# Performance work log

Hardware: AMD Instinct MI355X
Metric: run time of the kernel (lower is better)

The kernel has to match this reference:

```python
import math
import jax, jax.numpy as jnp
import numpy as np

B, N, D, H = 8, 512, 1024, 16
HD = D // H
K_DEFAULT, K_MAX, PROX_THR = 8, 12, 20.0


def setup_inputs() -> dict:
    key = jax.random.key(0)
    ks = jax.random.split(key, 12)
    tokens_B = jax.random.normal(ks[0], (B, N, D), dtype=jnp.float32)
    ego_distances = jax.random.uniform(ks[1], (B, N), dtype=jnp.float32)
    ego_mask = jnp.zeros((B, N), dtype=bool).at[:, 0].set(True)  # token 0 is ego
    ego_speed = jax.random.uniform(ks[2], (B,), dtype=jnp.float32)
    s = 1.0 / math.sqrt(D)
    Wq = jax.random.normal(ks[3], (D, D), jnp.float32) * s
    Wk = jax.random.normal(ks[4], (D, D), jnp.float32) * s
    Wv = jax.random.normal(ks[5], (D, D), jnp.float32) * s
    Weq = jax.random.normal(ks[6], (D, D), jnp.float32) * s
    Wo = jax.random.normal(ks[7], (D, D), jnp.float32) * (0.02 * s)
    Dm = D // 4
    W1 = jax.random.normal(ks[8], (Dm, 2), jnp.float32) * (1.0 / math.sqrt(2))
    b1 = jnp.zeros((Dm,), jnp.float32)
    W2 = jax.random.normal(ks[9], (H, Dm), jnp.float32) * (1.0 / math.sqrt(Dm))
    b2 = jnp.zeros((H,), jnp.float32)
    return dict(tokens_B=tokens_B, ego_distances=ego_distances, ego_mask=ego_mask,
                ego_speed=ego_speed, Wq=Wq, Wk=Wk, Wv=Wv, Weq=Weq, Wo=Wo,
                W1=W1, b1=b1, W2=W2, b2=b2)


def _compute_K(ego_speed, ego_distances):
    # deterministic, no-grad lookup (torch: @torch.no_grad)
    n = ego_distances.shape[1]
    close = (ego_distances < PROX_THR).astype(jnp.float32).sum(-1)
    density = close / max(n, 1)
    avg_speed = float(jnp.mean(ego_speed))
    avg_density = float(jnp.mean(density))
    K = K_DEFAULT
    if avg_speed > 15.0:
        K = min(K + 1, K_MAX)
    if avg_density > 0.5:
        K = min(K + 1, K_MAX)
    return min(K, n - 1)


def reference(tokens_B, ego_distances, ego_mask, ego_speed, Wq, Wk, Wv, Weq, Wo, W1, b1, W2, b2):
    b, n, d = tokens_B.shape
    K = _compute_K(ego_speed, ego_distances)
    if K <= 0:
        return jnp.zeros_like(tokens_B)

    # top-K nearest-to-ego neighbors per token, excluding self
    eye = jnp.eye(n, dtype=bool)
    dist_rank = jnp.where(eye[None, :, :], jnp.inf, ego_distances[:, None, :])  # (B,N,N)
    _, topk_idx = jax.lax.top_k(-dist_rank, K)  # (B,N,K) indices of smallest dists

    neighbors = jax.vmap(lambda t, idx: t[idx])(tokens_B, topk_idx)  # (B,N,K,D)

    is_ego = ego_mask.astype(tokens_B.dtype)[..., None]
    Q = (1.0 - is_ego) * (tokens_B @ Wq.T) + is_ego * (tokens_B @ Weq.T)
    Km = neighbors @ Wk.T
    Vm = neighbors @ Wv.T

    Q = Q.reshape(b, n, H, HD).transpose(0, 2, 1, 3)              # (B,H,N,hd)
    Km = Km.reshape(b, n, K, H, HD).transpose(0, 3, 1, 2, 4)      # (B,H,N,K,hd)
    Vm = Vm.reshape(b, n, K, H, HD).transpose(0, 3, 1, 2, 4)

    scores = jnp.einsum('bhnd,bhnkd->bhnk', Q, Km) / math.sqrt(HD)

    # additive pairwise distance bias MLP on (d_i_to_ego, d_j_to_ego)
    d_i = jnp.broadcast_to(ego_distances[:, :, None], (b, n, K))
    d_j = jax.vmap(lambda dd, idx: dd[idx])(ego_distances, topk_idx)
    dist_pair = jnp.stack([d_i, d_j], axis=-1)                    # (B,N,K,2)
    bias = jax.nn.relu(dist_pair @ W1.T + b1) @ W2.T + b2         # (B,N,K,H)
    scores = scores + bias.transpose(0, 3, 1, 2)                  # FIX-1: additive

    attn = jax.nn.softmax(scores, axis=-1)
    out = jnp.einsum('bhnk,bhnkd->bhnd', attn, Vm)
    out = out.transpose(0, 2, 1, 3).reshape(b, n, d)              # FIX-2 axis order
    return out @ Wo.T
```

## Files before the change

### kernel.cpp

```cpp
#include <hip/hip_runtime.h>
#include <math.h>

#define Bn 8
#define Nn 512
#define Dn 1024
#define Hn 16
#define HDn 64
#define KMAX 12
#define NSMAX 13
#define PROX 20.0f

typedef __attribute__((ext_vector_type(8))) short bf16x8;
typedef __attribute__((ext_vector_type(4))) float f32x4;

__device__ __forceinline__ unsigned short f2bf(float f) {
    unsigned int u = __float_as_uint(f);
    return (unsigned short)((u + 0x7FFFu + ((u >> 16) & 1u)) >> 16);
}

__global__ __launch_bounds__(256) void cvt_meta_kernel(const float* __restrict__ tokens,
                                                       const float* __restrict__ Wq,
                                                       const float* __restrict__ Wo,
                                                       const float* __restrict__ Wk,
                                                       const float* __restrict__ Wv,
                                                       const float* __restrict__ dist,
                                                       const float* __restrict__ speed,
                                                       unsigned short* __restrict__ tok_h,
                                                       unsigned short* __restrict__ wq_h,
                                                       unsigned short* __restrict__ wo_h,
                                                       unsigned short* __restrict__ wkv_h,
                                                       int* __restrict__ meta,
                                                       int* __restrict__ Lidx,
                                                       unsigned short* __restrict__ tok_g) {
    int blk = blockIdx.x;
    if (blk < 8192) {
        const float* src;
        unsigned short* dst;
        int local;
        if (blk < 4096) { src = tokens; dst = tok_h; local = blk; }
        else if (blk < 5120) { src = Wq; dst = wq_h; local = blk - 4096; }
        else if (blk < 6144) { src = Wo; dst = wo_h; local = blk - 5120; }
        else if (blk < 7168) { src = Wk; dst = wkv_h; local = blk - 6144; }
        else { src = Wv; dst = wkv_h + (size_t)Dn * Dn; local = blk - 7168; }
        int i = (local * 256 + threadIdx.x) * 4;
        float4 v = *(const float4*)&src[i];
        ushort4 o;
        o.x = f2bf(v.x); o.y = f2bf(v.y); o.z = f2bf(v.z); o.w = f2bf(v.w);
        *(ushort4*)&dst[i] = o;
        return;
    }
    if (threadIdx.x >= 64) return;
    int lane = threadIdx.x;
    int b = blk - 8192;

    int cnt = 0;
    for (int i = lane; i < Bn * Nn; i += 64) cnt += (dist[i] < PROX) ? 1 : 0;
    for (int off = 32; off; off >>= 1) cnt += __shfl_xor(cnt, off);

    float sp = 0.f;
    for (int i = lane; i < Bn; i += 64) sp += speed[i];
    for (int off = 32; off; off >>= 1) sp += __shfl_xor(sp, off);

    float avg_density = (float)cnt / (float)(Bn * Nn);
    float avg_speed = sp / (float)Bn;
    int K = 8;
    if (avg_speed > 15.0f) K = min(K + 1, KMAX);
    if (avg_density > 0.5f) K = min(K + 1, KMAX);
    K = min(K, Nn - 1);
    if (b == 0 && lane == 0) meta[0] = K;
    int ns = K + 1;

    int sel[NSMAX];
    float dloc[Nn / 64];
    #pragma unroll
    for (int j = 0; j < Nn / 64; ++j) dloc[j] = dist[b * Nn + lane + 64 * j];
    for (int r = 0; r < ns; ++r) {
        float mv = 1e30f;
        int mi = 0;
        #pragma unroll
        for (int j = 0; j < Nn / 64; ++j) {
            if (dloc[j] < mv) { mv = dloc[j]; mi = lane + 64 * j; }
        }
        for (int off = 32; off; off >>= 1) {
            float ov = __shfl_xor(mv, off);
            int oi = __shfl_xor(mi, off);
            if (ov < mv || (ov == mv && oi < mi)) { mv = ov; mi = oi; }
        }
        sel[r] = mi;
        if (lane == 0) Lidx[b * NSMAX + r] = mi;
        if ((mi & 63) == lane) dloc[mi >> 6] = 1e30f;
    }

    const float* srcp = &tokens[(size_t)(b * Nn + sel[0]) * Dn];
    float4 pre[4];
    #pragma unroll
    for (int q = 0; q < 4; ++q) pre[q] = *(const float4*)&srcp[(q * 64 + lane) * 4];
    for (int s = 0; s < ns; ++s) {
        float4 cur[4];
        #pragma unroll
        for (int q = 0; q < 4; ++q) cur[q] = pre[q];
        if (s + 1 < ns) {
            srcp = &tokens[(size_t)(b * Nn + sel[s + 1]) * Dn];
            #pragma unroll
            for (int q = 0; q < 4; ++q) pre[q] = *(const float4*)&srcp[(q * 64 + lane) * 4];
        }
        unsigned short* dst = &tok_g[(size_t)(b * 16 + s) * Dn];
        #pragma unroll
        for (int q = 0; q < 4; ++q) {
            ushort4 o;
            o.x = f2bf(cur[q].x); o.y = f2bf(cur[q].y); o.z = f2bf(cur[q].z); o.w = f2bf(cur[q].w);
            *(ushort4*)&dst[(q * 64 + lane) * 4] = o;
        }
    }
}

__device__ __forceinline__ void gemm_body_s(const unsigned short* A,
                                            const unsigned short* Bm,
                                            float* Cf, unsigned short* Ch,
                                            int Nd, int Kd, int sA, int sB,
                                            int bm, int bn, int mode, int hh,
                                            unsigned short* As, unsigned short* Bs) {
    int t = threadIdx.x;
    int wave = t >> 6, lane = t & 63;
    int wm = wave >> 1, wn = wave & 1;

    int srow = lane >> 2;
    int skoff = (lane & 3) * 8;
    const unsigned short* Ag  = A  + (size_t)(bm + wave * 16 + srow) * sA + skoff;
    const unsigned short* Bg  = Bm + (size_t)(bn + wave * 32 + srow) * sB + skoff;
    const unsigned short* Bg2 = Bg + (size_t)16 * sB;

    f32x4 acc[2][4] = {};
    int fm = lane & 15;
    int fk = (lane >> 4) * 8;

    auto stage = [&](int buf) {
        unsigned short* AsW  = As + buf * 2048 + (wave * 16) * 32;
        unsigned short* BsW  = Bs + buf * 4096 + (wave * 32) * 32;
        __builtin_amdgcn_global_load_lds((const __attribute__((address_space(1))) void*)Ag,
                                         (__attribute__((address_space(3))) void*)AsW, 16, 0, 0);
        __builtin_amdgcn_global_load_lds((const __attribute__((address_space(1))) void*)Bg,
                                         (__attribute__((address_space(3))) void*)BsW, 16, 0, 0);
        __builtin_amdgcn_global_load_lds((const __attribute__((address_space(1))) void*)Bg2,
                                         (__attribute__((address_space(3))) void*)(BsW + 512), 16, 0, 0);
        Ag += 32; Bg += 32; Bg2 += 32;
    };

    int nsteps = Kd >> 5;
    stage(0);
    __syncthreads();
    int cur = 0;
    for (int s = 0; s < nsteps; ++s) {
        if (s + 1 < nsteps) stage(cur ^ 1);
        const unsigned short* Ab = As + cur * 2048;
        const unsigned short* Bb = Bs + cur * 4096;
        bf16x8 af[2], bfr[4];
        #pragma unroll
        for (int mi = 0; mi < 2; ++mi)
            af[mi] = *(const bf16x8*)&Ab[(wm * 32 + mi * 16 + fm) * 32 + fk];
        #pragma unroll
        for (int ni = 0; ni < 4; ++ni)
            bfr[ni] = *(const bf16x8*)&Bb[(wn * 64 + ni * 16 + fm) * 32 + fk];
        #pragma unroll
        for (int mi = 0; mi < 2; ++mi)
            #pragma unroll
            for (int ni = 0; ni < 4; ++ni)
                acc[mi][ni] = __builtin_amdgcn_mfma_f32_16x16x32_bf16(af[mi], bfr[ni], acc[mi][ni], 0, 0, 0);
        __syncthreads();
        cur ^= 1;
    }

    int erow = (lane >> 4) * 4;
    #pragma unroll
    for (int mi = 0; mi < 2; ++mi)
        #pragma unroll
        for (int ni = 0; ni < 4; ++ni)
            #pragma unroll
            for (int r = 0; r < 4; ++r) {
                int row = bm + wm * 32 + mi * 16 + erow + r;
                int col = bn + wn * 64 + ni * 16 + fm;
                if (mode == 0) {
                    Cf[(size_t)row * Nd + col] = acc[mi][ni][r];
                } else if (mode == 1) {
                    Ch[(size_t)row * Nd + col] = f2bf(acc[mi][ni][r]);
                } else {
                    int bb = col >> 4, ss = col & 15;
                    Ch[((size_t)bb * 1024 + row) * 256 + ss * 16 + hh] = f2bf(acc[mi][ni][r]);
                }
            }
}

__global__ __launch_bounds__(256) void proj_fused_kernel(const unsigned short* __restrict__ tok_h,
                                                         const unsigned short* __restrict__ wq_h,
                                                         const unsigned short* __restrict__ tok_g,
                                                         const unsigned short* __restrict__ wkv_h,
                                                         const float* __restrict__ tokens,
                                                         const float* __restrict__ Weq,
                                                         float* __restrict__ Qbuf,
                                                         float* __restrict__ Kproj,
                                                         unsigned short* __restrict__ v_h,
                                                         float* __restrict__ Qego) {
    __shared__ unsigned short As[2 * 64 * 32];
    __shared__ unsigned short Bs[2 * 128 * 32];
    __shared__ float tok[Dn];

    int blk = blockIdx.x;
    if (blk < 16) {
        gemm_body_s(tok_g, wkv_h, Kproj, 0, Dn, Dn, Dn, Dn,
                    (blk >> 3) * 64, (blk & 7) * 128, 0, 0, As, Bs);
    } else if (blk < 32) {
        int idx = blk - 16;
        gemm_body_s(tok_g, wkv_h + (size_t)Dn * Dn, 0, v_h, Dn, Dn, Dn, Dn,
                    (idx >> 3) * 64, (idx & 7) * 128, 1, 0, As, Bs);
    } else if (blk < 544) {
        int idx = blk - 32;
        gemm_body_s(tok_h, wq_h, Qbuf, 0, Dn, Dn, Dn, Dn,
                    (idx >> 3) * 64, (idx & 7) * 128, 0, 0, As, Bs);
    } else {
        int blk2 = blk - 544;
        int b = blk2 >> 5, cg = blk2 & 31;
        for (int t = threadIdx.x; t < Dn; t += 256) tok[t] = tokens[(size_t)(b * Nn) * Dn + t];
        __syncthreads();
        int w = threadIdx.x >> 6, lane = threadIdx.x & 63;
        for (int o = 0; o < 8; ++o) {
            int col = cg * 32 + w * 8 + o;
            const float* wr = &Weq[(size_t)col * Dn];
            float sum = 0.f;
            #pragma unroll
            for (int q = 0; q < 4; ++q) {
                float4 w4 = *(const float4*)&wr[q * 256 + lane * 4];
                float4 t4 = *(const float4*)&tok[q * 256 + lane * 4];
                sum += w4.x * t4.x + w4.y * t4.y + w4.z * t4.z + w4.w * t4.w;
            }
            for (int off = 32; off; off >>= 1) sum += __shfl_xor(sum, off);
            if (lane == 0) Qego[(size_t)b * Dn + col] = sum;
        }
    }
}

__global__ __launch_bounds__(256) void vo3_gemm_kernel(const unsigned short* __restrict__ wo_h,
                                                       const unsigned short* __restrict__ v_h,
                                                       unsigned short* __restrict__ Vo3T) {
    __shared__ unsigned short As[2 * 64 * 32];
    __shared__ unsigned short Bs[2 * 128 * 32];
    int h = blockIdx.y;
    gemm_body_s(wo_h + h * HDn, v_h + h * HDn, 0, Vo3T, 0, HDn, Dn, Dn,
                blockIdx.x * 64, 0, 2, h, As, Bs);
}

#define HSTR 264
__global__ __launch_bounds__(256) void attn_kernel(const float* __restrict__ Q,
                                                   const float* __restrict__ Qego,
                                                   const float* __restrict__ Kproj,
                                                   const float* __restrict__ dist,
                                                   const float* __restrict__ W1,
                                                   const float* __restrict__ b1,
                                                   const float* __restrict__ W2,
                                                   const float* __restrict__ b2,
                                                   const int* __restrict__ meta,
                                                   const int* __restrict__ Lidx,
                                                   unsigned short* __restrict__ Wt) {
    __shared__ float hid[KMAX * HSTR];
    __shared__ float sc[Hn * NSMAX];
    __shared__ float at[Hn * NSMAX];
    __shared__ int selslot[NSMAX];
    __shared__ int inv[16];
    __shared__ float dj[NSMAX];

    int bi = blockIdx.x;
    int b = bi >> 9;
    int i = bi & (Nn - 1);
    int K = meta[0];
    int ns = K + 1;
    int t = threadIdx.x;
    int g = t >> 4, l = t & 15;

    float d_i = dist[b * Nn + i];

    const float* qsrc = (i == 0) ? &Qego[(size_t)b * Dn] : &Q[(size_t)bi * Dn];
    float4 qv = *(const float4*)&qsrc[g * HDn + l * 4];
    float4 w2v[4];
    #pragma unroll
    for (int ii = 0; ii < 4; ++ii)
        w2v[ii] = *(const float4*)&W2[g * 256 + ii * 64 + l * 4];

    if (t < 64) {
        int s = t;
        int jj = (s < ns) ? Lidx[b * NSMAX + s] : -1;
        bool valid = (s < ns) && (jj != i);
        unsigned long long mask = __ballot(valid);
        int rank = __popcll(mask & ((1ull << s) - 1ull));
        bool take = valid && (rank < K);
        if (take) {
            selslot[rank] = s;
            dj[rank] = dist[b * Nn + jj];
        }
        if (s < 16) inv[s] = take ? rank : -1;
    }
    __syncthreads();

    {
        float2 w01 = *(const float2*)&W1[2 * t];
        float bb = b1[t];
        for (int k = 0; k < K; ++k) {
            float h = w01.x * d_i + w01.y * dj[k] + bb;
            hid[k * HSTR + t] = h > 0.f ? h : 0.f;
        }
    }
    __syncthreads();

    {
        float bias0 = b2[g];
        float4 kvn = *(const float4*)&Kproj[(size_t)(b * 16 + selslot[0]) * Dn + g * HDn + l * 4];
        for (int k = 0; k < K; ++k) {
            float4 kv4 = kvn;
            if (k + 1 < K)
                kvn = *(const float4*)&Kproj[(size_t)(b * 16 + selslot[k + 1]) * Dn + g * HDn + l * 4];
            float val = (qv.x * kv4.x + qv.y * kv4.y + qv.z * kv4.z + qv.w * kv4.w) * 0.125f;
            #pragma unroll
            for (int ii = 0; ii < 4; ++ii) {
                float4 h4 = *(const float4*)&hid[k * HSTR + ii * 64 + l * 4];
                val += w2v[ii].x * h4.x + w2v[ii].y * h4.y + w2v[ii].z * h4.z + w2v[ii].w * h4.w;
            }
            val += __shfl_xor(val, 1);
            val += __shfl_xor(val, 2);
            val += __shfl_xor(val, 4);
            val += __shfl_xor(val, 8);
            if (l == 0) sc[g * NSMAX + k] = val + bias0;
        }
    }
    __syncthreads();

    {
        int k = l;
        float s = (k < K) ? sc[g * NSMAX + k] : -1e30f;
        float m = s;
        m = fmaxf(m, __shfl_xor(m, 1));
        m = fmaxf(m, __shfl_xor(m, 2));
        m = fmaxf(m, __shfl_xor(m, 4));
        m = fmaxf(m, __shfl_xor(m, 8));
        float e = (k < K) ? expf(s - m) : 0.f;
        float ssum = e;
        ssum += __shfl_xor(ssum, 1);
        ssum += __shfl_xor(ssum, 2);
        ssum += __shfl_xor(ssum, 4);
        ssum += __shfl_xor(ssum, 8);
        if (k < K) at[g * NSMAX + k] = e / ssum;
    }
    __syncthreads();

    {
        int s = t >> 4, h = t & 15;
        int k = (s < NSMAX) ? inv[s] : -1;
        float a = (k >= 0) ? at[h * NSMAX + k] : 0.f;
        Wt[(size_t)bi * 256 + t] = f2bf(a);
    }
}

__global__ __launch_bounds__(256) void final_gemm_kernel(const unsigned short* __restrict__ Wt,
                                                         const unsigned short* __restrict__ Vo3T,
                                                         float* __restrict__ out) {
    __shared__ unsigned short As[2 * 64 * 32];
    __shared__ unsigned short Bs[2 * 128 * 32];
    int rbase = blockIdx.y * 64;
    int b = rbase >> 9;
    int bmloc = rbase & (Nn - 1);
    gemm_body_s(Wt + (size_t)b * Nn * 256,
                Vo3T + (size_t)b * Dn * 256,
                out + (size_t)b * Nn * Dn, 0,
                Dn, 256, 256, 256, bmloc, blockIdx.x * 128, 0, 0, As, Bs);
}

extern "C" void kernel_launch(void* const* d_in, const int* in_sizes, int n_in,
                              void* d_out, int out_size, void* d_ws, size_t ws_size,
                              hipStream_t stream) {
    (void)in_sizes; (void)n_in; (void)out_size; (void)ws_size;
    const float* tokens = (const float*)d_in[0];
    const float* dist   = (const float*)d_in[1];
    const float* speed  = (const float*)d_in[3];
    const float* Wq  = (const float*)d_in[4];
    const float* Wk  = (const float*)d_in[5];
    const float* Wv  = (const float*)d_in[6];
    const float* Weq = (const float*)d_in[7];
    const float* Wo  = (const float*)d_in[8];
    const float* W1  = (const float*)d_in[9];
    const float* b1  = (const float*)d_in[10];
    const float* W2  = (const float*)d_in[11];
    const float* b2  = (const float*)d_in[12];
    float* out = (float*)d_out;

    char* ws = (char*)d_ws;
    const size_t SZ_KP   = (size_t)128 * Dn * sizeof(float);
    const size_t SZ_VH   = (size_t)128 * Dn * sizeof(unsigned short);
    const size_t SZ_V3   = (size_t)Bn * Dn * 256 * sizeof(unsigned short);
    const size_t SZ_WT   = (size_t)Bn * Nn * 256 * sizeof(unsigned short);
    const size_t SZ_BIG  = (size_t)Bn * Nn * Dn * sizeof(float);
    const size_t SZ_BIGH = (size_t)Bn * Nn * Dn * sizeof(unsigned short);
    const size_t SZ_WH   = (size_t)Dn * Dn * sizeof(unsigned short);
    const size_t SZ_TG   = (size_t)128 * Dn * sizeof(unsigned short);
    const size_t SZ_QE   = (size_t)Bn * Dn * sizeof(float);

    size_t off = 0;
    int*   meta  = (int*)(ws + off);  off += 256;
    int*   Lidx  = (int*)(ws + off);  off += 768;
    float* Kproj = (float*)(ws + off); off += SZ_KP;
    float* Qbuf  = (float*)(ws + off); off += SZ_BIG;
    float* Qego  = (float*)(ws + off); off += SZ_QE;
    unsigned short* v_h   = (unsigned short*)(ws + off); off += SZ_VH;
    unsigned short* Vo3T  = (unsigned short*)(ws + off); off += SZ_V3;
    unsigned short* Wt    = (unsigned short*)(ws + off); off += SZ_WT;
    unsigned short* tok_h = (unsigned short*)(ws + off); off += SZ_BIGH;
    unsigned short* wq_h  = (unsigned short*)(ws + off); off += SZ_WH;
    unsigned short* wo_h  = (unsigned short*)(ws + off); off += SZ_WH;
    unsigned short* wkv_h = (unsigned short*)(ws + off); off += 2 * SZ_WH;
    unsigned short* tok_g = (unsigned short*)(ws + off); off += SZ_TG;

    cvt_meta_kernel<<<8200, 256, 0, stream>>>(tokens, Wq, Wo, Wk, Wv, dist, speed,
                                              tok_h, wq_h, wo_h, wkv_h, meta, Lidx, tok_g);
    proj_fused_kernel<<<800, 256, 0, stream>>>(tok_h, wq_h, tok_g, wkv_h, tokens, Weq,
                                               Qbuf, Kproj, v_h, Qego);
    vo3_gemm_kernel<<<dim3(16, 16), 256, 0, stream>>>(wo_h, v_h, Vo3T);
    attn_kernel<<<Bn * Nn, 256, 0, stream>>>(Qbuf, Qego, Kproj, dist, W1, b1, W2, b2,
                                             meta, Lidx, Wt);
    final_gemm_kernel<<<dim3(Dn / 128, (Bn * Nn) / 64), 256, 0, stream>>>(Wt, Vo3T, out);
}
```

Before: 177.4 us.

## Store Q projection in bf16 and run attention with one wavefront per token

The Q projection GEMM now writes bf16 output instead of fp32, halving the Q buffer written by the projection and read by the attention kernel. The attention kernel is shrunk from 256 threads to a single 64-lane wavefront per token, which loops over heads and hidden units and drops all block barriers. It also switches to fast __expf and vectorized ushort4 stores of the attention weights. The risk is reduced Q precision and less parallelism per block, since each lane now handles four heads serially.

```diff
diff --git a/kernel.cpp b/kernel.cpp
--- a/kernel.cpp
+++ b/kernel.cpp
@@ -16,6 +16,9 @@
 __device__ __forceinline__ unsigned short f2bf(float f) {
     unsigned int u = __float_as_uint(f);
     return (unsigned short)((u + 0x7FFFu + ((u >> 16) & 1u)) >> 16);
+}
+__device__ __forceinline__ float bf2f(unsigned short u) {
+    return __uint_as_float(((unsigned int)u) << 16);
 }
 
 __global__ __launch_bounds__(256) void cvt_meta_kernel(const float* __restrict__ tokens,
@@ -196,7 +199,7 @@
                                                          const unsigned short* __restrict__ wkv_h,
                                                          const float* __restrict__ tokens,
                                                          const float* __restrict__ Weq,
-                                                         float* __restrict__ Qbuf,
+                                                         unsigned short* __restrict__ Qbuf_h,
                                                          float* __restrict__ Kproj,
                                                          unsigned short* __restrict__ v_h,
                                                          float* __restrict__ Qego) {
@@ -214,8 +217,8 @@
                     (idx >> 3) * 64, (idx & 7) * 128, 1, 0, As, Bs);
     } else if (blk < 544) {
         int idx = blk - 32;
-        gemm_body_s(tok_h, wq_h, Qbuf, 0, Dn, Dn, Dn, Dn,
-                    (idx >> 3) * 64, (idx & 7) * 128, 0, 0, As, Bs);
+        gemm_body_s(tok_h, wq_h, 0, Qbuf_h, Dn, Dn, Dn, Dn,
+                    (idx >> 3) * 64, (idx & 7) * 128, 1, 0, As, Bs);
     } else {
         int blk2 = blk - 544;
         int b = blk2 >> 5, cg = blk2 & 31;
@@ -249,17 +252,17 @@
 }
 
 #define HSTR 264
-__global__ __launch_bounds__(256) void attn_kernel(const float* __restrict__ Q,
-                                                   const float* __restrict__ Qego,
-                                                   const float* __restrict__ Kproj,
-                                                   const float* __restrict__ dist,
-                                                   const float* __restrict__ W1,
-                                                   const float* __restrict__ b1,
-                                                   const float* __restrict__ W2,
-                                                   const float* __restrict__ b2,
-                                                   const int* __restrict__ meta,
-                                                   const int* __restrict__ Lidx,
-                                                   unsigned short* __restrict__ Wt) {
+__global__ __launch_bounds__(64) void attn_kernel(const unsigned short* __restrict__ Qh,
+                                                  const float* __restrict__ Qego,
+                                                  const float* __restrict__ Kproj,
+                                                  const float* __restrict__ dist,
+                                                  const float* __restrict__ W1,
+                                                  const float* __restrict__ b1,
+                                                  const float* __restrict__ W2,
+                                                  const float* __restrict__ b2,
+                                                  const int* __restrict__ meta,
+                                                  const int* __restrict__ Lidx,
+                                                  unsigned short* __restrict__ Wt) {
     __shared__ float hid[KMAX * HSTR];
     __shared__ float sc[Hn * NSMAX];
     __shared__ float at[Hn * NSMAX];
@@ -272,20 +275,13 @@
     int i = bi & (Nn - 1);
     int K = meta[0];
     int ns = K + 1;
-    int t = threadIdx.x;
-    int g = t >> 4, l = t & 15;
+    int lane = threadIdx.x;
+    int gq = lane >> 4, l = lane & 15;
 
     float d_i = dist[b * Nn + i];
 
-    const float* qsrc = (i == 0) ? &Qego[(size_t)b * Dn] : &Q[(size_t)bi * Dn];
-    float4 qv = *(const float4*)&qsrc[g * HDn + l * 4];
-    float4 w2v[4];
-    #pragma unroll
-    for (int ii = 0; ii < 4; ++ii)
-        w2v[ii] = *(const float4*)&W2[g * 256 + ii * 64 + l * 4];
-
-    if (t < 64) {
-        int s = t;
+    {
+        int s = lane;
         int jj = (s < ns) ? Lidx[b * NSMAX + s] : -1;
         bool valid = (s < ns) && (jj != i);
         unsigned long long mask = __ballot(valid);
@@ -297,20 +293,33 @@
         }
         if (s < 16) inv[s] = take ? rank : -1;
     }
-    __syncthreads();
-
-    {
-        float2 w01 = *(const float2*)&W1[2 * t];
-        float bb = b1[t];
+
+    #pragma unroll
+    for (int j = 0; j < 4; ++j) {
+        int c = lane + 64 * j;
+        float2 w01 = *(const float2*)&W1[2 * c];
+        float bb = b1[c];
         for (int k = 0; k < K; ++k) {
             float h = w01.x * d_i + w01.y * dj[k] + bb;
-            hid[k * HSTR + t] = h > 0.f ? h : 0.f;
-        }
-    }
-    __syncthreads();
-
-    {
+            hid[k * HSTR + c] = h > 0.f ? h : 0.f;
+        }
+    }
+
+    for (int gg = 0; gg < 4; ++gg) {
+        int g = gq * 4 + gg;
+        float4 qv;
+        if (i == 0) {
+            qv = *(const float4*)&Qego[(size_t)b * Dn + g * HDn + l * 4];
+        } else {
+            ushort4 qh = *(const ushort4*)&Qh[(size_t)bi * Dn + g * HDn + l * 4];
+            qv.x = bf2f(qh.x); qv.y = bf2f(qh.y); qv.z = bf2f(qh.z); qv.w = bf2f(qh.w);
+        }
+        float4 w2v[4];
+        #pragma unroll
+        for (int ii = 0; ii < 4; ++ii)
+            w2v[ii] = *(const float4*)&W2[g * 256 + ii * 64 + l * 4];
         float bias0 = b2[g];
+
         float4 kvn = *(const float4*)&Kproj[(size_t)(b * 16 + selslot[0]) * Dn + g * HDn + l * 4];
         for (int k = 0; k < K; ++k) {
             float4 kv4 = kvn;
@@ -329,31 +338,38 @@
             if (l == 0) sc[g * NSMAX + k] = val + bias0;
         }
     }
-    __syncthreads();
-
-    {
+
+    #pragma unroll
+    for (int hh = 0; hh < 4; ++hh) {
+        int h = gq * 4 + hh;
         int k = l;
-        float s = (k < K) ? sc[g * NSMAX + k] : -1e30f;
+        float s = (k < K) ? sc[h * NSMAX + k] : -1e30f;
         float m = s;
         m = fmaxf(m, __shfl_xor(m, 1));
         m = fmaxf(m, __shfl_xor(m, 2));
         m = fmaxf(m, __shfl_xor(m, 4));
         m = fmaxf(m, __shfl_xor(m, 8));
-        float e = (k < K) ? expf(s - m) : 0.f;
+        float e = (k < K) ? __expf(s - m) : 0.f;
         float ssum = e;
         ssum += __shfl_xor(ssum, 1);
         ssum += __shfl_xor(ssum, 2);
         ssum += __shfl_xor(ssum, 4);
         ssum += __shfl_xor(ssum, 8);
-        if (k < K) at[g * NSMAX + k] = e / ssum;
-    }
-    __syncthreads();
+        if (k < K) at[h * NSMAX + k] = e / ssum;
+    }
 
     {
-        int s = t >> 4, h = t & 15;
-        int k = (s < NSMAX) ? inv[s] : -1;
-        float a = (k >= 0) ? at[h * NSMAX + k] : 0.f;
-        Wt[(size_t)bi * 256 + t] = f2bf(a);
+        ushort4 o;
+        unsigned short* op = (unsigned short*)&o;
+        #pragma unroll
+        for (int j = 0; j < 4; ++j) {
+            int tt = lane * 4 + j;
+            int s = tt >> 4, h = tt & 15;
+            int k = (s < NSMAX) ? inv[s] : -1;
+            float a = (k >= 0) ? at[h * NSMAX + k] : 0.f;
+            op[j] = f2bf(a);
+        }
+        *(ushort4*)&Wt[(size_t)bi * 256 + lane * 4] = o;
     }
 }
 
@@ -394,7 +410,7 @@
     const size_t SZ_VH   = (size_t)128 * Dn * sizeof(unsigned short);
     const size_t SZ_V3   = (size_t)Bn * Dn * 256 * sizeof(unsigned short);
     const size_t SZ_WT   = (size_t)Bn * Nn * 256 * sizeof(unsigned short);
-    const size_t SZ_BIG  = (size_t)Bn * Nn * Dn * sizeof(float);
+    const size_t SZ_QH   = (size_t)Bn * Nn * Dn * sizeof(unsigned short);
     const size_t SZ_BIGH = (size_t)Bn * Nn * Dn * sizeof(unsigned short);
     const size_t SZ_WH   = (size_t)Dn * Dn * sizeof(unsigned short);
     const size_t SZ_TG   = (size_t)128 * Dn * sizeof(unsigned short);
@@ -404,8 +420,8 @@
     int*   meta  = (int*)(ws + off);  off += 256;
     int*   Lidx  = (int*)(ws + off);  off += 768;
     float* Kproj = (float*)(ws + off); off += SZ_KP;
-    float* Qbuf  = (float*)(ws + off); off += SZ_BIG;
     float* Qego  = (float*)(ws + off); off += SZ_QE;
+    unsigned short* Qbuf_h = (unsigned short*)(ws + off); off += SZ_QH;
     unsigned short* v_h   = (unsigned short*)(ws + off); off += SZ_VH;
     unsigned short* Vo3T  = (unsigned short*)(ws + off); off += SZ_V3;
     unsigned short* Wt    = (unsigned short*)(ws + off); off += SZ_WT;
@@ -418,9 +434,9 @@
     cvt_meta_kernel<<<8200, 256, 0, stream>>>(tokens, Wq, Wo, Wk, Wv, dist, speed,
                                               tok_h, wq_h, wo_h, wkv_h, meta, Lidx, tok_g);
     proj_fused_kernel<<<800, 256, 0, stream>>>(tok_h, wq_h, tok_g, wkv_h, tokens, Weq,
-                                               Qbuf, Kproj, v_h, Qego);
+                                               Qbuf_h, Kproj, v_h, Qego);
     vo3_gemm_kernel<<<dim3(16, 16), 256, 0, stream>>>(wo_h, v_h, Vo3T);
-    attn_kernel<<<Bn * Nn, 256, 0, stream>>>(Qbuf, Qego, Kproj, dist, W1, b1, W2, b2,
-                                             meta, Lidx, Wt);
+    attn_kernel<<<Bn * Nn, 64, 0, stream>>>(Qbuf_h, Qego, Kproj, dist, W1, b1, W2, b2,
+                                            meta, Lidx, Wt);
     final_gemm_kernel<<<dim3(Dn / 128, (Bn * Nn) / 64), 256, 0, stream>>>(Wt, Vo3T, out);
 }
```

Result: slower. 196.3 us (+10.7%).
